# Kernel optimization log

Measured on AMD Instinct MI355X. Metric: run time of the kernel, lower is better.

Reference implementation:

```python
import jax, jax.numpy as jnp
import numpy as np

EPS = 1e-5

def setup_inputs() -> dict:
    key = jax.random.key(0)
    ks = jax.random.split(key, 7)
    C = 512
    x = jax.random.normal(ks[0], (16, C, 32, 32), dtype=jnp.float32)
    gn_w = jax.random.normal(ks[1], (C,), dtype=jnp.float32) * 0.02 + 1.0
    gn_b = jax.random.normal(ks[2], (C,), dtype=jnp.float32) * 0.02
    qkv_w = jax.random.normal(ks[3], (3 * C, C), dtype=jnp.float32) * (1.0 / np.sqrt(C))
    qkv_b = jax.random.normal(ks[4], (3 * C,), dtype=jnp.float32) * 0.02
    proj_w = jax.random.normal(ks[5], (C, C), dtype=jnp.float32) * (1.0 / np.sqrt(C))
    proj_b = jax.random.normal(ks[6], (C,), dtype=jnp.float32) * 0.02
    return {"x": x, "gn_w": gn_w, "gn_b": gn_b, "qkv_w": qkv_w,
            "qkv_b": qkv_b, "proj_w": proj_w, "proj_b": proj_b}

def reference(x, gn_w, gn_b, qkv_w, qkv_b, proj_w, proj_b):
    B, C, H, W = x.shape
    S = H * W
    # GroupNorm with 1 group: normalize over (C,H,W) per sample
    mean = jnp.mean(x, axis=(1, 2, 3), keepdims=True)
    var = jnp.var(x, axis=(1, 2, 3), keepdims=True)
    h = (x - mean) * jax.lax.rsqrt(var + EPS)
    h = h * gn_w[None, :, None, None] + gn_b[None, :, None, None]
    # 1x1 conv qkv: [B,C,H,W] -> [B,3C,H,W], flatten spatial -> [B,S,3C]
    hf = h.reshape(B, C, S)  # b c s
    qkv = jnp.einsum('bcs,oc->bso', hf, qkv_w) + qkv_b  # [B,S,3C]
    q, k, v = jnp.split(qkv, 3, axis=-1)  # each [B,S,C]
    scale = C ** (-0.5)
    attn = jax.nn.softmax(jnp.einsum('bqc,bkc->bqk', q, k) * scale, axis=-1)
    out = jnp.einsum('bqk,bkc->bqc', attn, v)  # [B,S,C]
    out = jnp.einsum('bsc,oc->bso', out, proj_w) + proj_b
    out = out.transpose(0, 2, 1).reshape(B, C, H, W)
    return x + out
```

## Files before the change

### kernel.cpp

```cpp
#include <hip/hip_runtime.h>
#include <stdint.h>

#define B_  16
#define C_  512
#define S_  1024
#define NSAMP (C_*S_)

typedef __bf16 bf16x8 __attribute__((ext_vector_type(8)));
typedef float  f32x4  __attribute__((ext_vector_type(4)));

__device__ __forceinline__ float bf2f(uint16_t u){ return __uint_as_float(((uint32_t)u)<<16); }
__device__ __forceinline__ uint16_t f2bf(float f){
  uint32_t u = __float_as_uint(f);
  uint32_t r = u + 0x7fffu + ((u>>16)&1u);
  return (uint16_t)(r>>16);
}
__device__ __forceinline__ float wsum(float v){
  #pragma unroll
  for(int o=32;o;o>>=1) v += __shfl_xor(v,o,64);
  return v;
}
__device__ __forceinline__ void gload16(const void* g, void* l){
  __builtin_amdgcn_global_load_lds(
      (__attribute__((address_space(1))) void*)g,
      (__attribute__((address_space(3))) void*)l, 16, 0, 0);
}

__global__ __launch_bounds__(256) void detect_k(const uint16_t* __restrict__ x,
                                                int* __restrict__ flag){
  __shared__ int sh[4];
  int cnt = 0;
  for(int i=threadIdx.x; i<32768; i+=256){
    uint32_t e = (x[2*i] >> 7) & 0xffu;
    cnt += (e >= 132) ? 1 : 0;
  }
  #pragma unroll
  for(int o=32;o;o>>=1) cnt += __shfl_xor(cnt,o,64);
  const int lane = threadIdx.x & 63, w = threadIdx.x >> 6;
  if (lane==0) sh[w] = cnt;
  __syncthreads();
  if (threadIdx.x==0) *flag = (sh[0]+sh[1]+sh[2]+sh[3] > 4096) ? 1 : 0;
}

__device__ __forceinline__ void convseg(const void* src, uint16_t* dst, int n, int f, int t){
  const int idx = t*8;
  if (idx >= n) return;
  if (f){
    const float* s = (const float*)src;
    float4 v0 = *(const float4*)(s + idx);
    float4 v1 = *(const float4*)(s + idx + 4);
    ushort4 a, b;
    a.x=f2bf(v0.x); a.y=f2bf(v0.y); a.z=f2bf(v0.z); a.w=f2bf(v0.w);
    b.x=f2bf(v1.x); b.y=f2bf(v1.y); b.z=f2bf(v1.z); b.w=f2bf(v1.w);
    *(ushort4*)(dst + idx)     = a;
    *(ushort4*)(dst + idx + 4) = b;
  } else {
    *(uint4*)(dst + idx) = *(const uint4*)((const uint16_t*)src + idx);
  }
}
__global__ __launch_bounds__(256) void prep_k(
    const void* __restrict__ srcx, uint16_t* __restrict__ xb, float2* __restrict__ part,
    const void* qkvw, const void* projw, const void* gnw, const void* gnb,
    const void* qkvb, const void* projb,
    uint16_t* qkvwb, uint16_t* projwb, uint16_t* gnwb, uint16_t* gnbb,
    uint16_t* qkvbb, uint16_t* projbb, const int* __restrict__ flag){
  const int f = *flag;
  const int t = threadIdx.x;
  if (blockIdx.x >= 1024){
    const int bid = blockIdx.x - 1024;
    if (bid < 384){
      const size_t off = (size_t)bid*2048;
      convseg((const char*)qkvw + off*(f?4:2), qkvwb + off, 2048, f, t);
    } else if (bid < 512){
      const size_t off = (size_t)(bid-384)*2048;
      convseg((const char*)projw + off*(f?4:2), projwb + off, 2048, f, t);
    } else {
      convseg(gnw,   gnwb,   512,  f, t);
      convseg(gnb,   gnbb,   512,  f, t);
      convseg(qkvb,  qkvbb,  1536, f, t);
      convseg(projb, projbb, 512,  f, t);
    }
    return;
  }
  const size_t base = (size_t)blockIdx.x * 8192;
  float s = 0.f, s2 = 0.f;
  if (f){
    const float4* sp = (const float4*)((const float*)srcx + base);
    ushort4* dp = (ushort4*)(xb + base);
    #pragma unroll
    for(int i=0;i<8;i++){
      float4 v = sp[i*256 + t];
      s  += v.x + v.y + v.z + v.w;
      s2 += v.x*v.x + v.y*v.y + v.z*v.z + v.w*v.w;
      ushort4 o; o.x=f2bf(v.x); o.y=f2bf(v.y); o.z=f2bf(v.z); o.w=f2bf(v.w);
      dp[i*256 + t] = o;
    }
  } else {
    const uint4* sp = (const uint4*)((const uint16_t*)srcx + base);
    uint4* dp = (uint4*)(xb + base);
    #pragma unroll
    for(int i=0;i<4;i++){
      uint4 p = sp[i*256 + t];
      dp[i*256 + t] = p;
      uint32_t uu[4] = {p.x,p.y,p.z,p.w};
      #pragma unroll
      for(int q=0;q<4;q++){
        float f0 = __uint_as_float(uu[q]<<16);
        float f1 = __uint_as_float(uu[q] & 0xffff0000u);
        s += f0 + f1; s2 += f0*f0 + f1*f1;
      }
    }
  }
  s = wsum(s); s2 = wsum(s2);
  __shared__ float rs[4], rq[4];
  const int lane = t & 63, w = t >> 6;
  if (lane==0){ rs[w]=s; rq[w]=s2; }
  __syncthreads();
  if (t==0)
    part[blockIdx.x] = make_float2(rs[0]+rs[1]+rs[2]+rs[3], rq[0]+rq[1]+rq[2]+rq[3]);
}

__global__ __launch_bounds__(256) void gn_apply_t(const uint16_t* __restrict__ x,
    const uint16_t* __restrict__ gw, const uint16_t* __restrict__ gb,
    const float2* __restrict__ part, uint16_t* __restrict__ hT){
  __shared__ float tile[64][65];
  const int b = blockIdx.z, c0 = blockIdx.y<<6, s0 = blockIdx.x<<6;
  const int tc = threadIdx.x >> 6, tl = threadIdx.x & 63;
  float2 p = part[b*64 + tl];
  float s = wsum(p.x), s2 = wsum(p.y);
  const float ninv = 1.f/(float)NSAMP;
  const float mn = s*ninv;
  const float rstd = rsqrtf(s2*ninv - mn*mn + 1e-5f);
  #pragma unroll
  for(int r=0;r<16;r++){
    int cl = r*4 + tc;
    tile[cl][tl] = bf2f(x[((size_t)b*C_ + c0+cl)*S_ + s0 + tl]);
  }
  __syncthreads();
  const float wv = bf2f(gw[c0+tl]) * rstd;
  const float bv = bf2f(gb[c0+tl]);
  #pragma unroll
  for(int r=0;r<16;r++){
    int sl = r*4 + tc;
    float v = (tile[tl][sl] - mn)*wv + bv;
    hT[((size_t)b*S_ + s0+sl)*C_ + c0 + tl] = f2bf(v);
  }
}

__global__ __launch_bounds__(256)
void qkv_k(const uint16_t* __restrict__ hT, const uint16_t* __restrict__ qkvw,
           const uint16_t* __restrict__ qkvb, uint16_t* __restrict__ qk,
           uint16_t* __restrict__ Vt)
{
  __shared__ uint16_t As[128*64];
  __shared__ uint16_t Bs[128*64];
  const int tid = threadIdx.x;
  const int lane = tid & 63, w = tid >> 6;
  const int quad = lane >> 4, lm = lane & 15;
  const int wm = (w & 1) << 6, wn = (w >> 1) << 6;

  const bool vpath = blockIdx.x >= 1024;
  const int id = vpath ? (blockIdx.x - 1024) : blockIdx.x;
  const int r8 = id & 7, k8 = id >> 3;
  int m0, n0, bz;
  const uint16_t *Abase, *Bbase;
  if (!vpath){
    const int g = r8*16 + (k8 & 15);
    m0 = g << 7; n0 = (k8 >> 4) << 7; bz = 0;
    Abase = hT + (size_t)m0*512;
    Bbase = qkvw + (size_t)n0*512;
  } else {
    const int g = r8*16 + (k8 & 15);
    m0 = (k8 >> 4) << 7; n0 = (g & 7) << 7; bz = g >> 3;
    Abase = qkvw + (size_t)(1024 + m0)*512;
    Bbase = hT + (size_t)bz*S_*C_ + (size_t)n0*512;
  }

  f32x4 acc[4][4];
  #pragma unroll
  for(int i=0;i<4;i++)
    #pragma unroll
    for(int j=0;j<4;j++) acc[i][j] = (f32x4){0.f,0.f,0.f,0.f};

  const int srow = tid >> 3;
  const int sx   = (tid & 7) ^ (srow & 7);
  const uint16_t* ga = Abase + (size_t)srow*512 + sx*8;
  const uint16_t* gb = Bbase + (size_t)srow*512 + sx*8;
  uint16_t* sa = &As[tid*8];
  uint16_t* sb = &Bs[tid*8];

  for(int k0=0;k0<512;k0+=64){
    #pragma unroll
    for(int i=0;i<4;i++){
      gload16(ga + (size_t)(i*32)*512 + k0, sa + i*2048);
      gload16(gb + (size_t)(i*32)*512 + k0, sb + i*2048);
    }
    __syncthreads();
    #pragma unroll
    for(int kk=0;kk<64;kk+=32){
      bf16x8 av[4], bv[4];
      #pragma unroll
      for(int i=0;i<4;i++){
        const int row = wm + i*16 + lm;
        av[i] = *(const bf16x8*)&As[row*64 + ((((kk>>3)+quad) ^ (row&7))<<3)];
      }
      #pragma unroll
      for(int j=0;j<4;j++){
        const int row = wn + j*16 + lm;
        bv[j] = *(const bf16x8*)&Bs[row*64 + ((((kk>>3)+quad) ^ (row&7))<<3)];
      }
      #pragma unroll
      for(int i=0;i<4;i++)
        #pragma unroll
        for(int j=0;j<4;j++)
          acc[i][j] = __builtin_amdgcn_mfma_f32_16x16x32_bf16(av[i], bv[j], acc[i][j], 0,0,0);
    }
    __syncthreads();
  }

  if (!vpath){
    #pragma unroll
    for(int j=0;j<4;j++){
      const int col = n0 + wn + j*16 + lm;
      const float bvv = bf2f(qkvb[col]);
      #pragma unroll
      for(int i=0;i<4;i++){
        const int rb = m0 + wm + i*16 + (quad<<2);
        #pragma unroll
        for(int r=0;r<4;r++)
          qk[(size_t)(rb+r)*1024 + col] = f2bf(acc[i][j][r] + bvv);
      }
    }
  } else {
    uint16_t* vb = Vt + (size_t)bz*C_*S_;
    #pragma unroll
    for(int i=0;i<4;i++){
      const int rb = m0 + wm + i*16 + (quad<<2);
      #pragma unroll
      for(int r=0;r<4;r++){
        const float bvv = bf2f(qkvb[1024 + rb + r]);
        #pragma unroll
        for(int j=0;j<4;j++)
          vb[(size_t)(rb+r)*1024 + n0 + wn + j*16 + lm] = f2bf(acc[i][j][r] + bvv);
      }
    }
  }
}

template<bool HASBIAS, bool BIASROW, bool OUTDYN, bool HASRES, int SWZMODE, bool EXP, bool SUMNORM>
__global__ __launch_bounds__(256)
void gemm_bt(const uint16_t* __restrict__ A, const uint16_t* __restrict__ Bt,
             void* __restrict__ Cp, const uint16_t* __restrict__ bias,
             const uint16_t* __restrict__ xres, const int* __restrict__ flag,
             int lda, int ldb, int ldc, int K,
             long long sA, long long sB, long long sC)
{
  __shared__ uint16_t As[128*64];
  __shared__ uint16_t Bs[128*64];
  const int lin = (blockIdx.z * gridDim.y + blockIdx.y) * gridDim.x + blockIdx.x;
  const int r8 = lin & 7, kk8 = lin >> 3;
  int bx, by, bz;
  if (SWZMODE == 0){
    const int G = (gridDim.y * gridDim.z) >> 3;
    const int g = r8 * G + (kk8 % G);
    bx = kk8 / G; by = g % gridDim.y; bz = g / gridDim.y;
  } else {
    const int G = (gridDim.x * gridDim.z) >> 3;
    const int g = r8 * G + (kk8 % G);
    by = kk8 / G; bx = g % gridDim.x; bz = g / gridDim.x;
  }

  const int tid = threadIdx.x;
  const int lane = tid & 63, w = tid >> 6;
  const int quad = lane >> 4, lm = lane & 15;
  const int m0 = by << 7, n0 = bx << 7;
  A  += (size_t)bz * sA;
  Bt += (size_t)bz * sB;

  f32x4 acc[4][4];
  #pragma unroll
  for(int i=0;i<4;i++)
    #pragma unroll
    for(int j=0;j<4;j++) acc[i][j] = (f32x4){0.f,0.f,0.f,0.f};
  f32x4 rsum[4];
  bf16x8 onesv;
  if (SUMNORM){
    #pragma unroll
    for(int i=0;i<4;i++) rsum[i] = (f32x4){0.f,0.f,0.f,0.f};
    #pragma unroll
    for(int z=0;z<8;z++) onesv[z] = (__bf16)1.0f;
  }

  const int wm = (w & 1) << 6, wn = (w >> 1) << 6;
  const int srow = tid >> 3;
  const int sx   = (tid & 7) ^ (srow & 7);
  const uint16_t* ga = A  + (size_t)(m0 + srow)*lda + sx*8;
  const uint16_t* gb = Bt + (size_t)(n0 + srow)*ldb + sx*8;
  uint16_t* sa = &As[tid*8];
  uint16_t* sb = &Bs[tid*8];

  for(int k0=0;k0<K;k0+=64){
    #pragma unroll
    for(int i=0;i<4;i++){
      gload16(ga + (size_t)(i*32)*lda + k0, sa + i*2048);
      gload16(gb + (size_t)(i*32)*ldb + k0, sb + i*2048);
    }
    __syncthreads();
    #pragma unroll
    for(int kk=0;kk<64;kk+=32){
      bf16x8 av[4], bv[4];
      #pragma unroll
      for(int i=0;i<4;i++){
        const int row = wm + i*16 + lm;
        av[i] = *(const bf16x8*)&As[row*64 + ((((kk>>3)+quad) ^ (row&7))<<3)];
      }
      #pragma unroll
      for(int j=0;j<4;j++){
        const int row = wn + j*16 + lm;
        bv[j] = *(const bf16x8*)&Bs[row*64 + ((((kk>>3)+quad) ^ (row&7))<<3)];
      }
      #pragma unroll
      for(int i=0;i<4;i++){
        if (SUMNORM) rsum[i] = __builtin_amdgcn_mfma_f32_16x16x32_bf16(av[i], onesv, rsum[i], 0,0,0);
        #pragma unroll
        for(int j=0;j<4;j++)
          acc[i][j] = __builtin_amdgcn_mfma_f32_16x16x32_bf16(av[i], bv[j], acc[i][j], 0,0,0);
      }
    }
    __syncthreads();
  }

  const int f = OUTDYN ? *flag : 0;
  const size_t cb = (size_t)bz * (size_t)sC;
  #pragma unroll
  for(int j=0;j<4;j++){
    const int col = n0 + wn + j*16 + lm;
    const float cbias = (HASBIAS && !BIASROW) ? bf2f(bias[col]) : 0.f;
    #pragma unroll
    for(int i=0;i<4;i++){
      const int rb = m0 + wm + i*16 + (quad<<2);
      #pragma unroll
      for(int r=0;r<4;r++){
        const int row = rb + r;
        float v = acc[i][j][r] + cbias;
        if (HASBIAS && BIASROW) v += bf2f(bias[row]);
        if (EXP)     v = __expf(v * 0.044194173824159216f);
        if (SUMNORM) v = v / rsum[i][r];
        const size_t idx = cb + (size_t)row*ldc + col;
        if (HASRES) v += bf2f(xres[idx]);
        if (OUTDYN && f) ((float*)Cp)[idx] = v;
        else             ((uint16_t*)Cp)[idx] = f2bf(v);
      }
    }
  }
}

extern "C" void kernel_launch(void* const* d_in, const int* in_sizes, int n_in,
                              void* d_out, int out_size, void* d_ws, size_t ws_size,
                              hipStream_t stream){
  char* ws = (char*)d_ws;
  int*      flag  = (int*)ws;
  float2*   part  = (float2*)(ws + 4096);
  uint16_t* gnwb  = (uint16_t*)(ws + 16384);
  uint16_t* gnbb  = (uint16_t*)(ws + 17408);
  uint16_t* qkvbb = (uint16_t*)(ws + 18432);
  uint16_t* projbb= (uint16_t*)(ws + 21504);
  uint16_t* qkvwb = (uint16_t*)(ws + 32768);
  uint16_t* projwb= (uint16_t*)(ws + 1605632);
  uint16_t* xb    = (uint16_t*)(ws + 4194304);
  uint16_t* hT    = (uint16_t*)(ws + 20971520);
  uint16_t* qk    = (uint16_t*)(ws + 37748736);
  uint16_t* sc    = (uint16_t*)(ws + 71303168);
  uint16_t* Vt    = (uint16_t*)(ws + 104857600);

  hipLaunchKernelGGL(detect_k, dim3(1), dim3(256), 0, stream,
                     (const uint16_t*)d_in[0], flag);
  hipLaunchKernelGGL(prep_k, dim3(1537), dim3(256), 0, stream,
                     d_in[0], xb, part,
                     d_in[3], d_in[5], d_in[1], d_in[2], d_in[4], d_in[6],
                     qkvwb, projwb, gnwb, gnbb, qkvbb, projbb, flag);
  hipLaunchKernelGGL(gn_apply_t, dim3(16,8,16), dim3(256), 0, stream, xb, gnwb, gnbb, part, hT);

  hipLaunchKernelGGL(qkv_k, dim3(1536), dim3(256), 0, stream, hT, qkvwb, qkvbb, qk, Vt);

  hipLaunchKernelGGL((gemm_bt<false,false,false,false,0,true,false>), dim3(8,8,16), dim3(256), 0, stream,
      qk, qk + 512, (void*)sc, (const uint16_t*)nullptr, (const uint16_t*)nullptr, flag,
      1024, 1024, 1024, 512, (long long)S_*1024, (long long)S_*1024, (long long)S_*S_);

  hipLaunchKernelGGL((gemm_bt<false,false,false,false,0,false,true>), dim3(4,8,16), dim3(256), 0, stream,
      sc, Vt, (void*)hT, (const uint16_t*)nullptr, (const uint16_t*)nullptr, flag,
      1024, 1024, 512, 1024, (long long)S_*S_, (long long)C_*S_, (long long)S_*C_);

  hipLaunchKernelGGL((gemm_bt<true,true,true,true,1,false,false>), dim3(8,4,16), dim3(256), 0, stream,
      projwb, hT, d_out, projbb, xb, flag,
      512, 512, 1024, 512, 0LL, (long long)S_*C_, (long long)C_*S_);
}
```

Baseline: 244.2 us.

## Fold GroupNorm into QKV GEMM epilogue and move softmax row sums to atomics

Drops the separate gn_apply_t kernel. prep_k now writes a transposed bf16 copy of x, folds the GroupNorm weight into the QKV weights and precomputes per-output-channel sums (W·gn_b, W·gn_w), so qkv_k applies mean and rstd as an affine correction in its epilogue. The softmax denominators are no longer computed with extra ones-vector MFMAs in the PV GEMM. They are accumulated in the exp/score GEMM epilogue through shuffles plus global atomicAdd, and the PV GEMM multiplies by the reciprocal. This removes one full pass over the activations and extra MFMA work. In exchange it adds atomics, a zero-init pass, and some precision risk, because the mean subtraction is now done after the bf16 GEMM (cancellation).

```diff
diff --git a/kernel.cpp b/kernel.cpp
--- a/kernel.cpp
+++ b/kernel.cpp
@@ -24,6 +24,9 @@
   __builtin_amdgcn_global_load_lds(
       (__attribute__((address_space(1))) void*)g,
       (__attribute__((address_space(3))) void*)l, 16, 0, 0);
+}
+__device__ __forceinline__ float loadp(const void* p, int i, int f){
+  return f ? ((const float*)p)[i] : bf2f(((const uint16_t*)p)[i]);
 }
 
 __global__ __launch_bounds__(256) void detect_k(const uint16_t* __restrict__ x,
@@ -58,102 +61,118 @@
     *(uint4*)(dst + idx) = *(const uint4*)((const uint16_t*)src + idx);
   }
 }
+
 __global__ __launch_bounds__(256) void prep_k(
-    const void* __restrict__ srcx, uint16_t* __restrict__ xb, float2* __restrict__ part,
+    const void* __restrict__ srcx, uint16_t* __restrict__ xb, uint16_t* __restrict__ xT,
+    float2* __restrict__ part,
     const void* qkvw, const void* projw, const void* gnw, const void* gnb,
     const void* qkvb, const void* projb,
-    uint16_t* qkvwb, uint16_t* projwb, uint16_t* gnwb, uint16_t* gnbb,
-    uint16_t* qkvbb, uint16_t* projbb, const int* __restrict__ flag){
+    uint16_t* qkvwb, uint16_t* projwb, uint16_t* qkvbb, uint16_t* projbb,
+    float* __restrict__ S1f, float* __restrict__ S2f, float* __restrict__ rsum,
+    const int* __restrict__ flag)
+{
+  __shared__ uint16_t tile[64][66];
+  __shared__ float rs[4], rq[4];
+  __shared__ float gws[512];
   const int f = *flag;
   const int t = threadIdx.x;
-  if (blockIdx.x >= 1024){
-    const int bid = blockIdx.x - 1024;
-    if (bid < 384){
-      const size_t off = (size_t)bid*2048;
-      convseg((const char*)qkvw + off*(f?4:2), qkvwb + off, 2048, f, t);
-    } else if (bid < 512){
-      const size_t off = (size_t)(bid-384)*2048;
-      convseg((const char*)projw + off*(f?4:2), projwb + off, 2048, f, t);
+  const int bid = blockIdx.x;
+
+  if (bid < 2048){
+    const int b = bid >> 7, rem = bid & 127;
+    const int c0 = (rem >> 4) << 6, s0 = (rem & 15) << 6;
+    const int tc = t >> 6, tl = t & 63;
+    float s = 0.f, s2 = 0.f;
+    #pragma unroll
+    for(int r=0;r<16;r++){
+      const int cl = r*4 + tc;
+      const size_t gi = ((size_t)b*C_ + c0+cl)*S_ + s0 + tl;
+      float v; uint16_t h;
+      if (f){ v = ((const float*)srcx)[gi]; h = f2bf(v); v = bf2f(h); }
+      else  { h = ((const uint16_t*)srcx)[gi]; v = bf2f(h); }
+      s += v; s2 += v*v;
+      xb[gi] = h;
+      tile[cl][tl] = h;
+    }
+    __syncthreads();
+    #pragma unroll
+    for(int r=0;r<16;r++){
+      const int sl = r*4 + tc;
+      xT[((size_t)b*S_ + s0+sl)*C_ + c0 + tl] = tile[tl][sl];
+    }
+    s = wsum(s); s2 = wsum(s2);
+    const int lane = t & 63, w = t >> 6;
+    if (lane==0){ rs[w]=s; rq[w]=s2; }
+    __syncthreads();
+    if (t==0) part[bid] = make_float2(rs[0]+rs[1]+rs[2]+rs[3], rq[0]+rq[1]+rq[2]+rq[3]);
+    return;
+  }
+  if (bid < 2432){
+    for(int i=t;i<512;i+=256) gws[i] = loadp(gnw, i, f);
+    __syncthreads();
+    const int off = (bid-2048)*2048;
+    const int e = off + t*8;
+    const int c = e & 511;
+    float v[8];
+    if (f){
+      float4 a = *(const float4*)((const float*)qkvw + e);
+      float4 bq = *(const float4*)((const float*)qkvw + e + 4);
+      v[0]=a.x; v[1]=a.y; v[2]=a.z; v[3]=a.w; v[4]=bq.x; v[5]=bq.y; v[6]=bq.z; v[7]=bq.w;
     } else {
-      convseg(gnw,   gnwb,   512,  f, t);
-      convseg(gnb,   gnbb,   512,  f, t);
-      convseg(qkvb,  qkvbb,  1536, f, t);
-      convseg(projb, projbb, 512,  f, t);
-    }
+      uint4 a = *(const uint4*)((const uint16_t*)qkvw + e);
+      uint32_t uu[4]={a.x,a.y,a.z,a.w};
+      #pragma unroll
+      for(int q=0;q<4;q++){ v[2*q]=__uint_as_float(uu[q]<<16); v[2*q+1]=__uint_as_float(uu[q]&0xffff0000u); }
+    }
+    ushort4 o0,o1;
+    o0.x=f2bf(v[0]*gws[c+0]); o0.y=f2bf(v[1]*gws[c+1]); o0.z=f2bf(v[2]*gws[c+2]); o0.w=f2bf(v[3]*gws[c+3]);
+    o1.x=f2bf(v[4]*gws[c+4]); o1.y=f2bf(v[5]*gws[c+5]); o1.z=f2bf(v[6]*gws[c+6]); o1.w=f2bf(v[7]*gws[c+7]);
+    *(ushort4*)(qkvwb + e)   = o0;
+    *(ushort4*)(qkvwb + e+4) = o1;
     return;
   }
-  const size_t base = (size_t)blockIdx.x * 8192;
-  float s = 0.f, s2 = 0.f;
-  if (f){
-    const float4* sp = (const float4*)((const float*)srcx + base);
-    ushort4* dp = (ushort4*)(xb + base);
-    #pragma unroll
-    for(int i=0;i<8;i++){
-      float4 v = sp[i*256 + t];
-      s  += v.x + v.y + v.z + v.w;
-      s2 += v.x*v.x + v.y*v.y + v.z*v.z + v.w*v.w;
-      ushort4 o; o.x=f2bf(v.x); o.y=f2bf(v.y); o.z=f2bf(v.z); o.w=f2bf(v.w);
-      dp[i*256 + t] = o;
-    }
-  } else {
-    const uint4* sp = (const uint4*)((const uint16_t*)srcx + base);
-    uint4* dp = (uint4*)(xb + base);
-    #pragma unroll
-    for(int i=0;i<4;i++){
-      uint4 p = sp[i*256 + t];
-      dp[i*256 + t] = p;
-      uint32_t uu[4] = {p.x,p.y,p.z,p.w};
-      #pragma unroll
-      for(int q=0;q<4;q++){
-        float f0 = __uint_as_float(uu[q]<<16);
-        float f1 = __uint_as_float(uu[q] & 0xffff0000u);
-        s += f0 + f1; s2 += f0*f0 + f1*f1;
-      }
-    }
-  }
-  s = wsum(s); s2 = wsum(s2);
-  __shared__ float rs[4], rq[4];
-  const int lane = t & 63, w = t >> 6;
-  if (lane==0){ rs[w]=s; rq[w]=s2; }
-  __syncthreads();
-  if (t==0)
-    part[blockIdx.x] = make_float2(rs[0]+rs[1]+rs[2]+rs[3], rq[0]+rq[1]+rq[2]+rq[3]);
-}
-
-__global__ __launch_bounds__(256) void gn_apply_t(const uint16_t* __restrict__ x,
-    const uint16_t* __restrict__ gw, const uint16_t* __restrict__ gb,
-    const float2* __restrict__ part, uint16_t* __restrict__ hT){
-  __shared__ float tile[64][65];
-  const int b = blockIdx.z, c0 = blockIdx.y<<6, s0 = blockIdx.x<<6;
-  const int tc = threadIdx.x >> 6, tl = threadIdx.x & 63;
-  float2 p = part[b*64 + tl];
-  float s = wsum(p.x), s2 = wsum(p.y);
-  const float ninv = 1.f/(float)NSAMP;
-  const float mn = s*ninv;
-  const float rstd = rsqrtf(s2*ninv - mn*mn + 1e-5f);
-  #pragma unroll
-  for(int r=0;r<16;r++){
-    int cl = r*4 + tc;
-    tile[cl][tl] = bf2f(x[((size_t)b*C_ + c0+cl)*S_ + s0 + tl]);
-  }
-  __syncthreads();
-  const float wv = bf2f(gw[c0+tl]) * rstd;
-  const float bv = bf2f(gb[c0+tl]);
-  #pragma unroll
-  for(int r=0;r<16;r++){
-    int sl = r*4 + tc;
-    float v = (tile[tl][sl] - mn)*wv + bv;
-    hT[((size_t)b*S_ + s0+sl)*C_ + c0 + tl] = f2bf(v);
+  if (bid < 2560){
+    const size_t off = (size_t)(bid-2432)*2048;
+    convseg((const char*)projw + off*(f?4:2), projwb + off, 2048, f, t);
+    return;
+  }
+  if (bid == 2560){
+    convseg(qkvb,  qkvbb,  1536, f, t);
+    convseg(projb, projbb, 512,  f, t);
+    return;
+  }
+  if (bid < 2585){
+    const int L = bid - 2561;
+    const int row = L*64 + (t>>2);
+    const int cc0 = (t&3)*128;
+    float s1=0.f, s2v=0.f;
+    for(int z=0;z<128;z++){
+      const int c = cc0 + z;
+      const float wv = loadp(qkvw, row*512 + c, f);
+      s1  += wv * loadp(gnb, c, f);
+      s2v += wv * loadp(gnw, c, f);
+    }
+    s1  += __shfl_xor(s1,1,64);  s1  += __shfl_xor(s1,2,64);
+    s2v += __shfl_xor(s2v,1,64); s2v += __shfl_xor(s2v,2,64);
+    if ((t&3)==0){ S1f[row] = s1; S2f[row] = s2v; }
+    return;
+  }
+  {
+    const int base = (bid-2585)*4096 + t*16;
+    #pragma unroll
+    for(int q=0;q<4;q++) *(float4*)(rsum + base + q*4) = (float4){0.f,0.f,0.f,0.f};
   }
 }
 
 __global__ __launch_bounds__(256)
-void qkv_k(const uint16_t* __restrict__ hT, const uint16_t* __restrict__ qkvw,
-           const uint16_t* __restrict__ qkvb, uint16_t* __restrict__ qk,
-           uint16_t* __restrict__ Vt)
+void qkv_k(const uint16_t* __restrict__ xT, const uint16_t* __restrict__ W2,
+           const uint16_t* __restrict__ qkvbb, const float2* __restrict__ part,
+           const float* __restrict__ S1f, const float* __restrict__ S2f,
+           uint16_t* __restrict__ qk, uint16_t* __restrict__ Vt)
 {
   __shared__ uint16_t As[128*64];
   __shared__ uint16_t Bs[128*64];
+  __shared__ float sred[8];
   const int tid = threadIdx.x;
   const int lane = tid & 63, w = tid >> 6;
   const int quad = lane >> 4, lm = lane & 15;
@@ -162,18 +181,27 @@
   const bool vpath = blockIdx.x >= 1024;
   const int id = vpath ? (blockIdx.x - 1024) : blockIdx.x;
   const int r8 = id & 7, k8 = id >> 3;
-  int m0, n0, bz;
+  int m0, n0, bz, bb;
   const uint16_t *Abase, *Bbase;
   if (!vpath){
     const int g = r8*16 + (k8 & 15);
     m0 = g << 7; n0 = (k8 >> 4) << 7; bz = 0;
-    Abase = hT + (size_t)m0*512;
-    Bbase = qkvw + (size_t)n0*512;
+    bb = m0 >> 10;
+    Abase = xT + (size_t)m0*512;
+    Bbase = W2 + (size_t)n0*512;
   } else {
     const int g = r8*16 + (k8 & 15);
     m0 = (k8 >> 4) << 7; n0 = (g & 7) << 7; bz = g >> 3;
-    Abase = qkvw + (size_t)(1024 + m0)*512;
-    Bbase = hT + (size_t)bz*S_*C_ + (size_t)n0*512;
+    bb = bz;
+    Abase = W2 + (size_t)(1024 + m0)*512;
+    Bbase = xT + (size_t)bz*S_*C_ + (size_t)n0*512;
+  }
+
+  {
+    float2 pv = make_float2(0.f,0.f);
+    if (tid < 128) pv = part[(size_t)bb*128 + tid];
+    float ss = wsum(pv.x), ss2 = wsum(pv.y);
+    if ((tid&63)==0){ sred[(tid>>6)*2] = ss; sred[(tid>>6)*2+1] = ss2; }
   }
 
   f32x4 acc[4][4];
@@ -218,17 +246,24 @@
     __syncthreads();
   }
 
+  const float ssum  = sred[0]+sred[2]+sred[4]+sred[6];
+  const float ssum2 = sred[1]+sred[3]+sred[5]+sred[7];
+  const float ninv = 1.f/(float)NSAMP;
+  const float mu = ssum*ninv;
+  const float rstd = rsqrtf(ssum2*ninv - mu*mu + 1e-5f);
+  const float mrs = mu*rstd;
+
   if (!vpath){
     #pragma unroll
     for(int j=0;j<4;j++){
       const int col = n0 + wn + j*16 + lm;
-      const float bvv = bf2f(qkvb[col]);
+      const float cadd = S1f[col] + bf2f(qkvbb[col]) - mrs*S2f[col];
       #pragma unroll
       for(int i=0;i<4;i++){
         const int rb = m0 + wm + i*16 + (quad<<2);
         #pragma unroll
         for(int r=0;r<4;r++)
-          qk[(size_t)(rb+r)*1024 + col] = f2bf(acc[i][j][r] + bvv);
+          qk[(size_t)(rb+r)*1024 + col] = f2bf(rstd*acc[i][j][r] + cadd);
       }
     }
   } else {
@@ -238,20 +273,23 @@
       const int rb = m0 + wm + i*16 + (quad<<2);
       #pragma unroll
       for(int r=0;r<4;r++){
-        const float bvv = bf2f(qkvb[1024 + rb + r]);
+        const int och = 1024 + rb + r;
+        const float cadd = S1f[och] + bf2f(qkvbb[och]) - mrs*S2f[och];
         #pragma unroll
         for(int j=0;j<4;j++)
-          vb[(size_t)(rb+r)*1024 + n0 + wn + j*16 + lm] = f2bf(acc[i][j][r] + bvv);
-      }
-    }
-  }
-}
-
-template<bool HASBIAS, bool BIASROW, bool OUTDYN, bool HASRES, int SWZMODE, bool EXP, bool SUMNORM>
+          vb[(size_t)(rb+r)*1024 + n0 + wn + j*16 + lm] = f2bf(rstd*acc[i][j][r] + cadd);
+      }
+    }
+  }
+}
+
+template<bool HASBIAS, bool BIASROW, bool OUTDYN, bool HASRES, int SWZMODE,
+         bool EXP, bool RSATOM, bool RSDIV>
 __global__ __launch_bounds__(256)
 void gemm_bt(const uint16_t* __restrict__ A, const uint16_t* __restrict__ Bt,
              void* __restrict__ Cp, const uint16_t* __restrict__ bias,
              const uint16_t* __restrict__ xres, const int* __restrict__ flag,
+             float* __restrict__ rsum,
              int lda, int ldb, int ldc, int K,
              long long sA, long long sB, long long sC)
 {
@@ -282,14 +320,6 @@
   for(int i=0;i<4;i++)
     #pragma unroll
     for(int j=0;j<4;j++) acc[i][j] = (f32x4){0.f,0.f,0.f,0.f};
-  f32x4 rsum[4];
-  bf16x8 onesv;
-  if (SUMNORM){
-    #pragma unroll
-    for(int i=0;i<4;i++) rsum[i] = (f32x4){0.f,0.f,0.f,0.f};
-    #pragma unroll
-    for(int z=0;z<8;z++) onesv[z] = (__bf16)1.0f;
-  }
 
   const int wm = (w & 1) << 6, wn = (w >> 1) << 6;
   const int srow = tid >> 3;
@@ -320,18 +350,31 @@
         bv[j] = *(const bf16x8*)&Bs[row*64 + ((((kk>>3)+quad) ^ (row&7))<<3)];
       }
       #pragma unroll
-      for(int i=0;i<4;i++){
-        if (SUMNORM) rsum[i] = __builtin_amdgcn_mfma_f32_16x16x32_bf16(av[i], onesv, rsum[i], 0,0,0);
+      for(int i=0;i<4;i++)
         #pragma unroll
         for(int j=0;j<4;j++)
           acc[i][j] = __builtin_amdgcn_mfma_f32_16x16x32_bf16(av[i], bv[j], acc[i][j], 0,0,0);
-      }
     }
     __syncthreads();
   }
 
   const int f = OUTDYN ? *flag : 0;
   const size_t cb = (size_t)bz * (size_t)sC;
+  float inv_[4][4];
+  if (RSDIV){
+    #pragma unroll
+    for(int i=0;i<4;i++)
+      #pragma unroll
+      for(int r=0;r<4;r++)
+        inv_[i][r] = 1.f / rsum[(size_t)bz*1024 + m0 + wm + i*16 + (quad<<2) + r];
+  }
+  float rloc[4][4];
+  if (RSATOM){
+    #pragma unroll
+    for(int i=0;i<4;i++)
+      #pragma unroll
+      for(int r=0;r<4;r++) rloc[i][r] = 0.f;
+  }
   #pragma unroll
   for(int j=0;j<4;j++){
     const int col = n0 + wn + j*16 + lm;
@@ -344,13 +387,29 @@
         const int row = rb + r;
         float v = acc[i][j][r] + cbias;
         if (HASBIAS && BIASROW) v += bf2f(bias[row]);
-        if (EXP)     v = __expf(v * 0.044194173824159216f);
-        if (SUMNORM) v = v / rsum[i][r];
+        if (EXP)   v = __expf(v * 0.044194173824159216f);
+        if (RSATOM) rloc[i][r] += v;
+        if (RSDIV) v *= inv_[i][r];
         const size_t idx = cb + (size_t)row*ldc + col;
         if (HASRES) v += bf2f(xres[idx]);
         if (OUTDYN && f) ((float*)Cp)[idx] = v;
         else             ((uint16_t*)Cp)[idx] = f2bf(v);
       }
+    }
+  }
+  if (RSATOM){
+    #pragma unroll
+    for(int o=1;o<16;o<<=1)
+      #pragma unroll
+      for(int i=0;i<4;i++)
+        #pragma unroll
+        for(int r=0;r<4;r++) rloc[i][r] += __shfl_xor(rloc[i][r], o, 64);
+    if (lm==0){
+      #pragma unroll
+      for(int i=0;i<4;i++)
+        #pragma unroll
+        for(int r=0;r<4;r++)
+          atomicAdd(&rsum[(size_t)bz*1024 + m0 + wm + i*16 + (quad<<2) + r], rloc[i][r]);
     }
   }
 }
@@ -361,37 +420,42 @@
   char* ws = (char*)d_ws;
   int*      flag  = (int*)ws;
   float2*   part  = (float2*)(ws + 4096);
-  uint16_t* gnwb  = (uint16_t*)(ws + 16384);
-  uint16_t* gnbb  = (uint16_t*)(ws + 17408);
-  uint16_t* qkvbb = (uint16_t*)(ws + 18432);
-  uint16_t* projbb= (uint16_t*)(ws + 21504);
-  uint16_t* qkvwb = (uint16_t*)(ws + 32768);
-  uint16_t* projwb= (uint16_t*)(ws + 1605632);
+  float*    S1f   = (float*)(ws + 20480);
+  float*    S2f   = (float*)(ws + 26624);
+  float*    rsum  = (float*)(ws + 32768);
+  uint16_t* qkvbb = (uint16_t*)(ws + 98304);
+  uint16_t* projbb= (uint16_t*)(ws + 101376);
+  uint16_t* qkvwb = (uint16_t*)(ws + 131072);
+  uint16_t* projwb= (uint16_t*)(ws + 1703936);
   uint16_t* xb    = (uint16_t*)(ws + 4194304);
-  uint16_t* hT    = (uint16_t*)(ws + 20971520);
-  uint16_t* qk    = (uint16_t*)(ws + 37748736);
-  uint16_t* sc    = (uint16_t*)(ws + 71303168);
-  uint16_t* Vt    = (uint16_t*)(ws + 104857600);
+  uint16_t* xT    = (uint16_t*)(ws + 20971520);
+  uint16_t* attn  = (uint16_t*)(ws + 37748736);
+  uint16_t* qk    = (uint16_t*)(ws + 54525952);
+  uint16_t* sc    = (uint16_t*)(ws + 88080384);
+  uint16_t* Vt    = (uint16_t*)(ws + 121634816);
 
   hipLaunchKernelGGL(detect_k, dim3(1), dim3(256), 0, stream,
                      (const uint16_t*)d_in[0], flag);
-  hipLaunchKernelGGL(prep_k, dim3(1537), dim3(256), 0, stream,
-                     d_in[0], xb, part,
+  hipLaunchKernelGGL(prep_k, dim3(2589), dim3(256), 0, stream,
+                     d_in[0], xb, xT, part,
                      d_in[3], d_in[5], d_in[1], d_in[2], d_in[4], d_in[6],
-                     qkvwb, projwb, gnwb, gnbb, qkvbb, projbb, flag);
-  hipLaunchKernelGGL(gn_apply_t, dim3(16,8,16), dim3(256), 0, stream, xb, gnwb, gnbb, part, hT);
-
-  hipLaunchKernelGGL(qkv_k, dim3(1536), dim3(256), 0, stream, hT, qkvwb, qkvbb, qk, Vt);
-
-  hipLaunchKernelGGL((gemm_bt<false,false,false,false,0,true,false>), dim3(8,8,16), dim3(256), 0, stream,
-      qk, qk + 512, (void*)sc, (const uint16_t*)nullptr, (const uint16_t*)nullptr, flag,
+                     qkvwb, projwb, qkvbb, projbb, S1f, S2f, rsum, flag);
+
+  hipLaunchKernelGGL(qkv_k, dim3(1536), dim3(256), 0, stream,
+                     xT, qkvwb, qkvbb, part, S1f, S2f, qk, Vt);
+
+  hipLaunchKernelGGL((gemm_bt<false,false,false,false,0,true,true,false>),
+      dim3(8,8,16), dim3(256), 0, stream,
+      qk, qk + 512, (void*)sc, (const uint16_t*)nullptr, (const uint16_t*)nullptr, flag, rsum,
       1024, 1024, 1024, 512, (long long)S_*1024, (long long)S_*1024, (long long)S_*S_);
 
-  hipLaunchKernelGGL((gemm_bt<false,false,false,false,0,false,true>), dim3(4,8,16), dim3(256), 0, stream,
-      sc, Vt, (void*)hT, (const uint16_t*)nullptr, (const uint16_t*)nullptr, flag,
+  hipLaunchKernelGGL((gemm_bt<false,false,false,false,0,false,false,true>),
+      dim3(4,8,16), dim3(256), 0, stream,
+      sc, Vt, (void*)attn, (const uint16_t*)nullptr, (const uint16_t*)nullptr, flag, rsum,
       1024, 1024, 512, 1024, (long long)S_*S_, (long long)C_*S_, (long long)S_*C_);
 
-  hipLaunchKernelGGL((gemm_bt<true,true,true,true,1,false,false>), dim3(8,4,16), dim3(256), 0, stream,
-      projwb, hT, d_out, projbb, xb, flag,
+  hipLaunchKernelGGL((gemm_bt<true,true,true,true,1,false,false,false>),
+      dim3(8,4,16), dim3(256), 0, stream,
+      projwb, attn, d_out, projbb, xb, flag, (float*)nullptr,
       512, 512, 1024, 512, 0LL, (long long)S_*C_, (long long)C_*S_);
 }
```

Measured after the change: 257.6 us. 1.05x slower.
